# Performance work log

Measured on AMD Instinct MI355X. Metric: run time of the kernel, lower is better.

The kernel has to match this reference:

```python
import jax, jax.numpy as jnp
import numpy as np

K = 4096          # num_embeddings
D = 256           # embedding_dim
COMMIT = 0.25     # commitment_cost


def setup_inputs() -> dict:
    key = jax.random.key(0)
    k1, k2 = jax.random.split(key)
    z = jax.random.normal(k1, (16, D, 32, 32), dtype=jnp.float32)
    # codebook init: uniform(-1/K, 1/K) as in the torch module
    emb = jax.random.uniform(k2, (K, D), dtype=jnp.float32,
                             minval=-1.0 / K, maxval=1.0 / K)
    return {"z": z, "emb": emb}


def reference(z, emb):
    B, Dm, H, W = z.shape
    # (B, D, H, W) -> (B*H*W, D)
    z_flat = jnp.transpose(z, (0, 2, 3, 1)).reshape(-1, Dm)
    # squared L2 distances to every codebook vector: (N, K)
    distances = (jnp.sum(z_flat * z_flat, axis=1, keepdims=True)
                 + jnp.sum(emb * emb, axis=1)
                 - 2.0 * jnp.matmul(z_flat, emb.T))
    encoding_indices = jnp.argmin(distances, axis=1)            # (N,)
    encodings = jax.nn.one_hot(encoding_indices, emb.shape[0],
                               dtype=z.dtype)                   # (N, K)
    quantized = jnp.take(emb, encoding_indices, axis=0)         # == encodings @ emb

    sg = jax.lax.stop_gradient
    e_latent_loss = jnp.mean((sg(quantized) - z_flat) ** 2)
    q_latent_loss = jnp.mean((quantized - sg(z_flat)) ** 2)
    loss = q_latent_loss + COMMIT * e_latent_loss

    avg_probs = jnp.mean(encodings, axis=0)
    perplexity = jnp.exp(-jnp.sum(avg_probs * jnp.log(avg_probs + 1e-10)))

    # straight-through estimator
    quantized = z_flat + sg(quantized - z_flat)
    # NOTE: faithful to source: torch does .view(B, D, H, W) on the (N, D)
    # flat tensor WITHOUT permuting back -- a plain reshape, replicated here.
    quantized = quantized.reshape(B, Dm, H, W)
    return quantized, loss, perplexity, encodings
```

## Files before the change

kernel.cpp:

```cpp
#include <hip/hip_runtime.h>

#define NN 16384
#define KK 4096
#define DD 256

typedef __attribute__((ext_vector_type(8))) short short8;
typedef __attribute__((ext_vector_type(4))) float f32x4;

static __device__ __forceinline__ unsigned short f2bf(float f) {
  unsigned u = __float_as_uint(f);
  unsigned r = (u + 0x7FFFu + ((u >> 16) & 1u)) >> 16;
  return (unsigned short)r;
}

static __device__ __forceinline__ unsigned int mono(float f) {
  unsigned u = __float_as_uint(f);
  return (u & 0x80000000u) ? ~u : (u | 0x80000000u);
}

__global__ void vq_e2(const float* __restrict__ emb, float* __restrict__ e2g) {
  int k = blockIdx.x;
  int lane = threadIdx.x;
  float4 v = *reinterpret_cast<const float4*>(&emb[k * DD + lane * 4]);
  float s = v.x * v.x + v.y * v.y + v.z * v.z + v.w * v.w;
  #pragma unroll
  for (int o = 1; o < 64; o <<= 1) s += __shfl_xor(s, o);
  if (lane == 0) e2g[k] = s;
}

__global__ __launch_bounds__(256) void vq_scores(
    const float* __restrict__ z, const float* __restrict__ emb,
    const float* __restrict__ e2g, unsigned long long* __restrict__ keys) {
  __shared__ unsigned short zt[128][264];
  __shared__ unsigned short et[64][264];
  __shared__ float e2t[64];

  const int tid = threadIdx.x;
  const int bx = blockIdx.x;
  const int by = blockIdx.y;

  const long zbase = (long)(bx >> 3) * 262144 + (long)(bx & 7) * 128;
  {
    int n4 = (tid & 31) << 2;
    int dl = tid >> 5;
    for (int p = 0; p < 32; ++p) {
      int d = (p << 3) + dl;
      float4 v = *reinterpret_cast<const float4*>(&z[zbase + (long)d * 1024 + n4]);
      zt[n4 + 0][d] = f2bf(v.x);
      zt[n4 + 1][d] = f2bf(v.y);
      zt[n4 + 2][d] = f2bf(v.z);
      zt[n4 + 3][d] = f2bf(v.w);
    }
  }

  const int lane = tid & 63;
  const int wid = tid >> 6;
  const int l16 = lane & 15;
  const int g4 = lane >> 4;

  float bestv0 = INFINITY, bestv1 = INFINITY;
  int besti0 = 0, besti1 = 0;

  for (int kt = 0; kt < 16; ++kt) {
    __syncthreads();
    {
      const long ebase = ((long)by * 1024 + (long)kt * 64) * DD;
      for (int p = 0; p < 16; ++p) {
        int idx = (p << 8) + tid;
        int r = idx >> 6;
        int c4 = (idx & 63) << 2;
        float4 v = *reinterpret_cast<const float4*>(&emb[ebase + r * DD + c4]);
        ushort4 w;
        w.x = f2bf(v.x); w.y = f2bf(v.y); w.z = f2bf(v.z); w.w = f2bf(v.w);
        *reinterpret_cast<ushort4*>(&et[r][c4]) = w;
      }
      if (tid < 64) e2t[tid] = e2g[by * 1024 + kt * 64 + tid];
    }
    __syncthreads();

    f32x4 acc[4][2];
    #pragma unroll
    for (int m = 0; m < 4; ++m)
      #pragma unroll
      for (int r = 0; r < 2; ++r) acc[m][r] = (f32x4){0.f, 0.f, 0.f, 0.f};

    #pragma unroll
    for (int ds = 0; ds < 8; ++ds) {
      const int dcol = ds * 32 + g4 * 8;
      short8 a0 = *reinterpret_cast<const short8*>(&et[ 0 + l16][dcol]);
      short8 a1 = *reinterpret_cast<const short8*>(&et[16 + l16][dcol]);
      short8 a2 = *reinterpret_cast<const short8*>(&et[32 + l16][dcol]);
      short8 a3 = *reinterpret_cast<const short8*>(&et[48 + l16][dcol]);
      short8 b0 = *reinterpret_cast<const short8*>(&zt[wid * 32 + l16][dcol]);
      short8 b1 = *reinterpret_cast<const short8*>(&zt[wid * 32 + 16 + l16][dcol]);
      acc[0][0] = __builtin_amdgcn_mfma_f32_16x16x32_bf16(a0, b0, acc[0][0], 0, 0, 0);
      acc[0][1] = __builtin_amdgcn_mfma_f32_16x16x32_bf16(a0, b1, acc[0][1], 0, 0, 0);
      acc[1][0] = __builtin_amdgcn_mfma_f32_16x16x32_bf16(a1, b0, acc[1][0], 0, 0, 0);
      acc[1][1] = __builtin_amdgcn_mfma_f32_16x16x32_bf16(a1, b1, acc[1][1], 0, 0, 0);
      acc[2][0] = __builtin_amdgcn_mfma_f32_16x16x32_bf16(a2, b0, acc[2][0], 0, 0, 0);
      acc[2][1] = __builtin_amdgcn_mfma_f32_16x16x32_bf16(a2, b1, acc[2][1], 0, 0, 0);
      acc[3][0] = __builtin_amdgcn_mfma_f32_16x16x32_bf16(a3, b0, acc[3][0], 0, 0, 0);
      acc[3][1] = __builtin_amdgcn_mfma_f32_16x16x32_bf16(a3, b1, acc[3][1], 0, 0, 0);
    }

    #pragma unroll
    for (int m = 0; m < 4; ++m) {
      #pragma unroll
      for (int rg = 0; rg < 4; ++rg) {
        int krow = m * 16 + g4 * 4 + rg;
        float e2v = e2t[krow];
        int kk = by * 1024 + kt * 64 + krow;
        float s0 = fmaf(-2.0f, acc[m][0][rg], e2v);
        float s1 = fmaf(-2.0f, acc[m][1][rg], e2v);
        if (s0 < bestv0) { bestv0 = s0; besti0 = kk; }
        if (s1 < bestv1) { bestv1 = s1; besti1 = kk; }
      }
    }
  }

  unsigned long long key0 =
      ((unsigned long long)mono(bestv0) << 32) | (unsigned)besti0;
  unsigned long long key1 =
      ((unsigned long long)mono(bestv1) << 32) | (unsigned)besti1;
  unsigned long long o;
  o = __shfl_xor(key0, 16); if (o < key0) key0 = o;
  o = __shfl_xor(key0, 32); if (o < key0) key0 = o;
  o = __shfl_xor(key1, 16); if (o < key1) key1 = o;
  o = __shfl_xor(key1, 32); if (o < key1) key1 = o;
  if (g4 == 0) {
    int n0 = bx * 128 + wid * 32 + l16;
    atomicMin(&keys[n0], key0);
    atomicMin(&keys[n0 + 16], key1);
  }
}

__global__ __launch_bounds__(256) void vq_finish(
    const float* __restrict__ z, const float* __restrict__ emb,
    const unsigned long long* __restrict__ keys, unsigned int* __restrict__ counts,
    float* __restrict__ lossacc, float* __restrict__ outq, float* __restrict__ enc) {
  __shared__ float ztile[64][257];
  __shared__ int sidx[64];
  __shared__ float wsum[4];

  const int tid = threadIdx.x;
  const int n0 = blockIdx.x * 64;
  const long zbase = (long)(n0 >> 10) * 262144 + (long)(n0 & 1023);

  {
    int n4 = (tid & 15) << 2;
    int dl = tid >> 4;
    for (int p = 0; p < 16; ++p) {
      int d = p * 16 + dl;
      float4 v = *reinterpret_cast<const float4*>(&z[zbase + (long)d * 1024 + n4]);
      ztile[n4 + 0][d] = v.x;
      ztile[n4 + 1][d] = v.y;
      ztile[n4 + 2][d] = v.z;
      ztile[n4 + 3][d] = v.w;
    }
  }
  if (tid < 64) {
    int n = n0 + tid;
    int idx = (int)(keys[n] & 0xFFFFFFFFULL);
    sidx[tid] = idx;
    atomicAdd(&counts[idx], 1u);
    enc[(long)n * KK + idx] = 1.0f;
  }
  __syncthreads();

  float lacc = 0.f;
  const int d = tid;
  for (int nl = 0; nl < 64; ++nl) {
    int idx = sidx[nl];
    float e = emb[idx * DD + d];
    float zz = ztile[nl][d];
    float df = e - zz;
    lacc += df * df;
    outq[(long)(n0 + nl) * DD + d] = zz + (e - zz);
  }
  #pragma unroll
  for (int o = 1; o < 64; o <<= 1) lacc += __shfl_xor(lacc, o);
  if ((tid & 63) == 0) wsum[tid >> 6] = lacc;
  __syncthreads();
  if (tid == 0) atomicAdd(lossacc, wsum[0] + wsum[1] + wsum[2] + wsum[3]);
}

__global__ void vq_scalars(const unsigned int* __restrict__ counts,
                           const float* __restrict__ lossacc,
                           float* __restrict__ outs) {
  __shared__ double sh[256];
  int t = threadIdx.x;
  double ent = 0.0;
  for (int k = t; k < KK; k += 256) {
    double p = (double)counts[k] / (double)NN;
    ent += p * log(p + 1e-10);
  }
  sh[t] = ent;
  __syncthreads();
  for (int s = 128; s > 0; s >>= 1) {
    if (t < s) sh[t] += sh[t + s];
    __syncthreads();
  }
  if (t == 0) {
    outs[0] = lossacc[0] * 1.25f / ((float)NN * (float)DD);
    outs[1] = (float)exp(-sh[0]);
  }
}

extern "C" void kernel_launch(void* const* d_in, const int* in_sizes, int n_in,
                              void* d_out, int out_size, void* d_ws, size_t ws_size,
                              hipStream_t stream) {
  const float* z = (const float*)d_in[0];
  const float* emb = (const float*)d_in[1];
  float* out = (float*)d_out;
  float* outq = out;
  float* outs = out + 4194304;
  float* enc = out + 4194306;

  char* ws = (char*)d_ws;
  unsigned long long* keys = (unsigned long long*)ws;
  unsigned int* counts = (unsigned int*)(ws + 131072);
  float* lossacc = (float*)(ws + 147456);
  float* e2g = (float*)(ws + 147472);

  hipMemsetAsync(keys, 0xFF, 131072, stream);
  hipMemsetAsync(ws + 131072, 0, 16388, stream);
  hipMemsetAsync(enc, 0, (size_t)NN * KK * 4, stream);

  vq_e2<<<KK, 64, 0, stream>>>(emb, e2g);
  vq_scores<<<dim3(NN / 128, 4), 256, 0, stream>>>(z, emb, e2g, keys);
  vq_finish<<<NN / 64, 256, 0, stream>>>(z, emb, keys, counts, lossacc, outq, enc);
  vq_scalars<<<1, 256, 0, stream>>>(counts, lossacc, outs);
}
```

Measured before the change: 435.2 us.

## Pre-convert inputs to bf16 and use tiled 128x128 MFMA GEMM with direct LDS loads

Adds prep kernels that convert the codebook and the transposed z into bf16 buffers once, and computes the squared norms alongside. The distance kernel becomes a 128x128 block-tiled MFMA GEMM that loads tiles via global_load_lds and reduces the argmin through LDS before one atomic per row. This removes the repeated per-block fp32 to bf16 conversion and the transposed z staging, and raises data reuse per block. It costs extra workspace traffic for the bf16 copies, and the unpadded LDS tiles may cause bank conflicts.

```diff
diff --git a/kernel.cpp b/kernel.cpp
--- a/kernel.cpp
+++ b/kernel.cpp
@@ -9,8 +9,7 @@
 
 static __device__ __forceinline__ unsigned short f2bf(float f) {
   unsigned u = __float_as_uint(f);
-  unsigned r = (u + 0x7FFFu + ((u >> 16) & 1u)) >> 16;
-  return (unsigned short)r;
+  return (unsigned short)((u + 0x7FFFu + ((u >> 16) & 1u)) >> 16);
 }
 
 static __device__ __forceinline__ unsigned int mono(float f) {
@@ -18,119 +17,140 @@
   return (u & 0x80000000u) ? ~u : (u | 0x80000000u);
 }
 
-__global__ void vq_e2(const float* __restrict__ emb, float* __restrict__ e2g) {
-  int k = blockIdx.x;
-  int lane = threadIdx.x;
-  float4 v = *reinterpret_cast<const float4*>(&emb[k * DD + lane * 4]);
+__global__ __launch_bounds__(256) void vq_prep_emb(
+    const float* __restrict__ emb, unsigned short* __restrict__ eb,
+    float* __restrict__ e2g) {
+  const int wid = threadIdx.x >> 6, lane = threadIdx.x & 63;
+  const int row = blockIdx.x * 4 + wid;
+  float4 v = *reinterpret_cast<const float4*>(&emb[row * DD + lane * 4]);
+  ushort4 w;
+  w.x = f2bf(v.x); w.y = f2bf(v.y); w.z = f2bf(v.z); w.w = f2bf(v.w);
+  *reinterpret_cast<ushort4*>(&eb[row * DD + lane * 4]) = w;
   float s = v.x * v.x + v.y * v.y + v.z * v.z + v.w * v.w;
   #pragma unroll
   for (int o = 1; o < 64; o <<= 1) s += __shfl_xor(s, o);
-  if (lane == 0) e2g[k] = s;
-}
-
-__global__ __launch_bounds__(256) void vq_scores(
-    const float* __restrict__ z, const float* __restrict__ emb,
-    const float* __restrict__ e2g, unsigned long long* __restrict__ keys) {
-  __shared__ unsigned short zt[128][264];
-  __shared__ unsigned short et[64][264];
-  __shared__ float e2t[64];
-
+  if (lane == 0) e2g[row] = s;
+}
+
+__global__ __launch_bounds__(256) void vq_prep_z(
+    const float* __restrict__ z, unsigned short* __restrict__ zb) {
+  __shared__ unsigned short t[64][72];
   const int tid = threadIdx.x;
   const int bx = blockIdx.x;
-  const int by = blockIdx.y;
-
-  const long zbase = (long)(bx >> 3) * 262144 + (long)(bx & 7) * 128;
-  {
-    int n4 = (tid & 31) << 2;
-    int dl = tid >> 5;
-    for (int p = 0; p < 32; ++p) {
-      int d = (p << 3) + dl;
-      float4 v = *reinterpret_cast<const float4*>(&z[zbase + (long)d * 1024 + n4]);
-      zt[n4 + 0][d] = f2bf(v.x);
-      zt[n4 + 1][d] = f2bf(v.y);
-      zt[n4 + 2][d] = f2bf(v.z);
-      zt[n4 + 3][d] = f2bf(v.w);
-    }
-  }
-
-  const int lane = tid & 63;
-  const int wid = tid >> 6;
-  const int l16 = lane & 15;
-  const int g4 = lane >> 4;
-
-  float bestv0 = INFINITY, bestv1 = INFINITY;
-  int besti0 = 0, besti1 = 0;
-
-  for (int kt = 0; kt < 16; ++kt) {
+  const int b = bx >> 6, rem = bx & 63, dt = rem >> 4, ht = rem & 15;
+  const float* src = z + (long)b * 262144 + (long)dt * 64 * 1024 + ht * 64;
+  #pragma unroll
+  for (int p = 0; p < 16; ++p) {
+    int idx = p * 256 + tid;
+    int dl = idx >> 6, hl = idx & 63;
+    t[hl][dl] = f2bf(src[dl * 1024 + hl]);
+  }
+  __syncthreads();
+  unsigned short* dst = zb + ((long)b * 1024 + (long)ht * 64) * DD + dt * 64;
+  #pragma unroll
+  for (int p = 0; p < 2; ++p) {
+    int idx = p * 256 + tid;
+    int hl = idx >> 3, c8 = idx & 7;
+    short8 v = *reinterpret_cast<const short8*>(&t[hl][c8 * 8]);
+    *reinterpret_cast<short8*>(&dst[(long)hl * DD + c8 * 8]) = v;
+  }
+}
+
+__global__ __launch_bounds__(256) void vq_gemm(
+    const unsigned short* __restrict__ eb, const unsigned short* __restrict__ zb,
+    const float* __restrict__ e2g, unsigned long long* __restrict__ keys) {
+  __shared__ unsigned short At[128 * 64];
+  __shared__ unsigned short Bt[128 * 64];
+  __shared__ float e2s[128];
+  __shared__ unsigned long long wkey[2][128];
+
+  const int tid = threadIdx.x;
+  const int bm = blockIdx.x;
+  const int bn = blockIdx.y;
+  const int lane = tid & 63, wid = tid >> 6;
+  const int wm = wid >> 1, wn = wid & 1;
+  const int l16 = lane & 15, g4 = lane >> 4;
+
+  if (tid < 128) {
+    e2s[tid] = e2g[bm * 128 + tid];
+    wkey[0][tid] = ~0ull;
+    wkey[1][tid] = ~0ull;
+  }
+
+  const long abase = (long)bm * 128 * DD;
+  const long bbase = (long)bn * 128 * DD;
+
+  f32x4 acc[4][4];
+  #pragma unroll
+  for (int mi = 0; mi < 4; ++mi)
+    #pragma unroll
+    for (int ni = 0; ni < 4; ++ni) acc[mi][ni] = (f32x4){0.f, 0.f, 0.f, 0.f};
+
+  for (int kt = 0; kt < 4; ++kt) {
     __syncthreads();
     {
-      const long ebase = ((long)by * 1024 + (long)kt * 64) * DD;
-      for (int p = 0; p < 16; ++p) {
-        int idx = (p << 8) + tid;
-        int r = idx >> 6;
-        int c4 = (idx & 63) << 2;
-        float4 v = *reinterpret_cast<const float4*>(&emb[ebase + r * DD + c4]);
-        ushort4 w;
-        w.x = f2bf(v.x); w.y = f2bf(v.y); w.z = f2bf(v.z); w.w = f2bf(v.w);
-        *reinterpret_cast<ushort4*>(&et[r][c4]) = w;
+      const int lr = lane >> 3, lc = (lane & 7) * 8;
+      #pragma unroll
+      for (int c = 0; c < 4; ++c) {
+        const int row0 = wid * 32 + c * 8;
+        const unsigned short* ga =
+            eb + abase + (long)(row0 + lr) * DD + kt * 64 + lc;
+        __builtin_amdgcn_global_load_lds(
+            (const __attribute__((address_space(1))) void*)ga,
+            (__attribute__((address_space(3))) void*)&At[row0 * 64], 16, 0, 0);
+        const unsigned short* gb =
+            zb + bbase + (long)(row0 + lr) * DD + kt * 64 + lc;
+        __builtin_amdgcn_global_load_lds(
+            (const __attribute__((address_space(1))) void*)gb,
+            (__attribute__((address_space(3))) void*)&Bt[row0 * 64], 16, 0, 0);
       }
-      if (tid < 64) e2t[tid] = e2g[by * 1024 + kt * 64 + tid];
     }
     __syncthreads();
 
-    f32x4 acc[4][2];
     #pragma unroll
-    for (int m = 0; m < 4; ++m)
-      #pragma unroll
-      for (int r = 0; r < 2; ++r) acc[m][r] = (f32x4){0.f, 0.f, 0.f, 0.f};
-
+    for (int kk = 0; kk < 2; ++kk) {
+      short8 a[4], b[4];
+      #pragma unroll
+      for (int mi = 0; mi < 4; ++mi)
+        a[mi] = *reinterpret_cast<const short8*>(
+            &At[(wm * 64 + mi * 16 + l16) * 64 + kk * 32 + g4 * 8]);
+      #pragma unroll
+      for (int ni = 0; ni < 4; ++ni)
+        b[ni] = *reinterpret_cast<const short8*>(
+            &Bt[(wn * 64 + ni * 16 + l16) * 64 + kk * 32 + g4 * 8]);
+      #pragma unroll
+      for (int mi = 0; mi < 4; ++mi)
+        #pragma unroll
+        for (int ni = 0; ni < 4; ++ni)
+          acc[mi][ni] = __builtin_amdgcn_mfma_f32_16x16x32_bf16(
+              a[mi], b[ni], acc[mi][ni], 0, 0, 0);
+    }
+  }
+
+  #pragma unroll
+  for (int ni = 0; ni < 4; ++ni) {
+    float bv = INFINITY;
+    int bi = 0;
     #pragma unroll
-    for (int ds = 0; ds < 8; ++ds) {
-      const int dcol = ds * 32 + g4 * 8;
-      short8 a0 = *reinterpret_cast<const short8*>(&et[ 0 + l16][dcol]);
-      short8 a1 = *reinterpret_cast<const short8*>(&et[16 + l16][dcol]);
-      short8 a2 = *reinterpret_cast<const short8*>(&et[32 + l16][dcol]);
-      short8 a3 = *reinterpret_cast<const short8*>(&et[48 + l16][dcol]);
-      short8 b0 = *reinterpret_cast<const short8*>(&zt[wid * 32 + l16][dcol]);
-      short8 b1 = *reinterpret_cast<const short8*>(&zt[wid * 32 + 16 + l16][dcol]);
-      acc[0][0] = __builtin_amdgcn_mfma_f32_16x16x32_bf16(a0, b0, acc[0][0], 0, 0, 0);
-      acc[0][1] = __builtin_amdgcn_mfma_f32_16x16x32_bf16(a0, b1, acc[0][1], 0, 0, 0);
-      acc[1][0] = __builtin_amdgcn_mfma_f32_16x16x32_bf16(a1, b0, acc[1][0], 0, 0, 0);
-      acc[1][1] = __builtin_amdgcn_mfma_f32_16x16x32_bf16(a1, b1, acc[1][1], 0, 0, 0);
-      acc[2][0] = __builtin_amdgcn_mfma_f32_16x16x32_bf16(a2, b0, acc[2][0], 0, 0, 0);
-      acc[2][1] = __builtin_amdgcn_mfma_f32_16x16x32_bf16(a2, b1, acc[2][1], 0, 0, 0);
-      acc[3][0] = __builtin_amdgcn_mfma_f32_16x16x32_bf16(a3, b0, acc[3][0], 0, 0, 0);
-      acc[3][1] = __builtin_amdgcn_mfma_f32_16x16x32_bf16(a3, b1, acc[3][1], 0, 0, 0);
-    }
-
-    #pragma unroll
-    for (int m = 0; m < 4; ++m) {
-      #pragma unroll
-      for (int rg = 0; rg < 4; ++rg) {
-        int krow = m * 16 + g4 * 4 + rg;
-        float e2v = e2t[krow];
-        int kk = by * 1024 + kt * 64 + krow;
-        float s0 = fmaf(-2.0f, acc[m][0][rg], e2v);
-        float s1 = fmaf(-2.0f, acc[m][1][rg], e2v);
-        if (s0 < bestv0) { bestv0 = s0; besti0 = kk; }
-        if (s1 < bestv1) { bestv1 = s1; besti1 = kk; }
+    for (int mi = 0; mi < 4; ++mi) {
+      #pragma unroll
+      for (int r = 0; r < 4; ++r) {
+        int krow = wm * 64 + mi * 16 + g4 * 4 + r;
+        float s = fmaf(-2.0f, acc[mi][ni][r], e2s[krow]);
+        if (s < bv) { bv = s; bi = bm * 128 + krow; }
       }
     }
-  }
-
-  unsigned long long key0 =
-      ((unsigned long long)mono(bestv0) << 32) | (unsigned)besti0;
-  unsigned long long key1 =
-      ((unsigned long long)mono(bestv1) << 32) | (unsigned)besti1;
-  unsigned long long o;
-  o = __shfl_xor(key0, 16); if (o < key0) key0 = o;
-  o = __shfl_xor(key0, 32); if (o < key0) key0 = o;
-  o = __shfl_xor(key1, 16); if (o < key1) key1 = o;
-  o = __shfl_xor(key1, 32); if (o < key1) key1 = o;
-  if (g4 == 0) {
-    int n0 = bx * 128 + wid * 32 + l16;
-    atomicMin(&keys[n0], key0);
-    atomicMin(&keys[n0 + 16], key1);
+    unsigned long long key =
+        ((unsigned long long)mono(bv) << 32) | (unsigned)bi;
+    unsigned long long o;
+    o = __shfl_xor(key, 16); if (o < key) key = o;
+    o = __shfl_xor(key, 32); if (o < key) key = o;
+    if (g4 == 0) wkey[wm][wn * 64 + ni * 16 + l16] = key;
+  }
+  __syncthreads();
+  if (tid < 128) {
+    unsigned long long k0 = wkey[0][tid], k1 = wkey[1][tid];
+    atomicMin(&keys[(long)bn * 128 + tid], k0 < k1 ? k0 : k1);
   }
 }
 
@@ -217,17 +237,20 @@
   float* enc = out + 4194306;
 
   char* ws = (char*)d_ws;
-  unsigned long long* keys = (unsigned long long*)ws;
-  unsigned int* counts = (unsigned int*)(ws + 131072);
-  float* lossacc = (float*)(ws + 147456);
-  float* e2g = (float*)(ws + 147472);
+  unsigned short* zb = (unsigned short*)ws;
+  unsigned short* eb = (unsigned short*)(ws + 8388608);
+  float* e2g = (float*)(ws + 10485760);
+  unsigned long long* keys = (unsigned long long*)(ws + 10502144);
+  unsigned int* counts = (unsigned int*)(ws + 10633216);
+  float* lossacc = (float*)(ws + 10649600);
 
   hipMemsetAsync(keys, 0xFF, 131072, stream);
-  hipMemsetAsync(ws + 131072, 0, 16388, stream);
+  hipMemsetAsync(ws + 10633216, 0, 16388, stream);
   hipMemsetAsync(enc, 0, (size_t)NN * KK * 4, stream);
 
-  vq_e2<<<KK, 64, 0, stream>>>(emb, e2g);
-  vq_scores<<<dim3(NN / 128, 4), 256, 0, stream>>>(z, emb, e2g, keys);
+  vq_prep_emb<<<1024, 256, 0, stream>>>(emb, eb, e2g);
+  vq_prep_z<<<1024, 256, 0, stream>>>(z, zb);
+  vq_gemm<<<dim3(32, 128), 256, 0, stream>>>(eb, zb, e2g, keys);
   vq_finish<<<NN / 64, 256, 0, stream>>>(z, emb, keys, counts, lossacc, outq, enc);
   vq_scalars<<<1, 256, 0, stream>>>(counts, lossacc, outs);
 }
```

Result: faster. 396.4 us (-8.9%).
